# Kernel tuning notes

Hardware: AMD Instinct MI355X
Metric: run time of the kernel (lower is better)

Reference implementation:

```python
import jax, jax.numpy as jnp
from jax import lax
import numpy as np

N, I, O = 64, 8, 8
B = 512
S_EX, S_PHI, S_RHO = 10, 60, 60  # S_phi must equal S_rho (alpha loops feed S_rho-sized h into the GRUs)
N_ACTIONS, N_ROLES = 5, 7


def _gru(x, h, Wih, Whh, bih, bhh):
    # torch.nn.GRUCell math
    gi = x @ Wih.T + bih
    gh = h @ Whh.T + bhh
    ir, iz, inn = jnp.split(gi, 3, axis=-1)
    hr, hz, hn = jnp.split(gh, 3, axis=-1)
    r = jax.nn.sigmoid(ir + hr)
    zg = jax.nn.sigmoid(iz + hz)
    n = jnp.tanh(inn + r * hn)
    return (1.0 - zg) * n + zg * h


def setup_inputs() -> dict:
    key = jax.random.key(0)
    ks = jax.random.split(key, 24)
    f32 = jnp.float32
    z = jax.random.normal(ks[0], (B, N, S_EX), f32)
    dz = jax.random.normal(ks[1], (B, N, S_EX), f32)
    has = (jax.random.uniform(ks[2], (B, N)) < 0.9).astype(f32)
    adj = (jnp.triu(jax.random.uniform(ks[3], (N, N)), 1) > 0.7).astype(jnp.int32)

    def lin(k, o, i):
        return (jax.random.normal(k, (o, i), f32) * np.float32(1.0 / np.sqrt(i)))

    d = dict(z=z, dz=dz, has=has, adj=adj)
    d['Wih_f'] = lin(ks[4], 3 * S_PHI, S_RHO)
    d['Whh_f'] = lin(ks[5], 3 * S_PHI, S_PHI)
    d['bih_f'] = jax.random.normal(ks[6], (3 * S_PHI,), f32) * 0.02
    d['bhh_f'] = jax.random.normal(ks[7], (3 * S_PHI,), f32) * 0.02
    d['Wih_b'] = lin(ks[8], 3 * S_PHI, S_RHO)
    d['Whh_b'] = lin(ks[9], 3 * S_PHI, S_PHI)
    d['bih_b'] = jax.random.normal(ks[10], (3 * S_PHI,), f32) * 0.02
    d['bhh_b'] = jax.random.normal(ks[11], (3 * S_PHI,), f32) * 0.02
    d['Wf'] = lin(ks[12], S_RHO, S_PHI + 2 * S_EX)
    d['bf'] = jax.random.normal(ks[13], (S_RHO,), f32) * 0.02
    d['Wb'] = lin(ks[14], S_RHO, S_PHI + 2 * S_EX)
    d['bb'] = jax.random.normal(ks[15], (S_RHO,), f32) * 0.02
    d['Wa'] = lin(ks[16], N_ACTIONS, 2 * S_PHI)
    d['ba'] = jax.random.normal(ks[17], (N_ACTIONS,), f32) * 0.02
    d['Wc'] = lin(ks[18], 1, 2 * S_PHI)
    d['bc'] = jax.random.normal(ks[19], (1,), f32) * 0.02
    d['Wu'] = lin(ks[20], N_ROLES, 2 * S_RHO)
    d['bu'] = jax.random.normal(ks[21], (N_ROLES,), f32) * 0.02
    return d


def reference(z, dz, has, adj,
              Wih_f, Whh_f, bih_f, bhh_f,
              Wih_b, Whh_b, bih_b, bhh_b,
              Wf, bf, Wb, bb, Wa, ba, Wc, bc, Wu, bu):
    Bn, Nn = has.shape
    dt = z.dtype
    adjf = adj.astype(dt)

    # ---- forward sweep over nodes in ascending order ----
    def fwd_outer(rho, i):
        def inner(h, j):
            hn = _gru(rho[j], h, Wih_f, Whh_f, bih_f, bhh_f)
            blend = adjf[j, i] * has[:, j][:, None]  # edge exists AND source node present
            return h + blend * (hn - h), None
        h, _ = lax.scan(inner, jnp.zeros((Bn, S_PHI), dt), jnp.arange(Nn))
        rho_i = jnp.tanh(jnp.concatenate([h, z[:, i], dz[:, i]], 1) @ Wf.T + bf)
        return rho.at[i].set(rho_i), None

    rho_f, _ = lax.scan(fwd_outer, jnp.zeros((Nn, Bn, S_RHO), dt), jnp.arange(Nn))

    # ---- backward sweep over nodes in descending order ----
    def bwd_outer(rho, i):
        def inner(h, j):
            hn = _gru(rho[j], h, Wih_b, Whh_b, bih_b, bhh_b)
            blend = adjf[i, j] * has[:, j][:, None]  # out-edges of i, visited descending
            return h + blend * (hn - h), None
        h, _ = lax.scan(inner, jnp.zeros((Bn, S_PHI), dt), jnp.arange(Nn - 1, -1, -1))
        rho_i = jnp.concatenate([h, z[:, i], dz[:, i]], 1) @ Wb.T + bb
        return rho.at[i].set(rho_i), None

    rho_b, _ = lax.scan(bwd_outer, jnp.zeros((Nn, Bn, S_RHO), dt), jnp.arange(Nn - 1, -1, -1))

    # ---- aggregate outputs (last O nodes) and inputs (first I nodes) ----
    h = jnp.zeros((Bn, S_RHO), dt)
    for i in range(N - O, N):
        hn = _gru(rho_f[i], h, Wih_f, Whh_f, bih_f, bhh_f)
        h = h + has[:, i][:, None] * (hn - h)
    alpha_f = h
    h = jnp.zeros((Bn, S_RHO), dt)
    for i in reversed(range(I)):
        hn = _gru(rho_b[i], h, Wih_b, Whh_b, bih_b, bhh_b)
        h = h + has[:, i][:, None] * (hn - h)
    alpha_b = h

    ab = jnp.concatenate([alpha_f, alpha_b], 1)
    omega = ab @ Wa.T + ba          # [B, 5]
    value = ab @ Wc.T + bc          # [B, 1]

    feats = jnp.concatenate([rho_f, rho_b], -1)           # [N, B, 2*S_rho]
    psi = jnp.einsum('nbs,rs->brn', feats, Wu) + bu[None, :, None]  # [B, 7, N]
    m = has[:, None, :]
    psi = -60.0 * (1.0 - m) + psi * m  # interpolate(-60, psi, has)

    instr_prob = jax.nn.softmax(omega, axis=1)
    role_prob = jax.nn.softmax(psi, axis=2)
    return instr_prob, role_prob, value
```

## Files before the change

kernel.cpp:

```cpp
#include <hip/hip_runtime.h>
#include <hip/hip_bf16.h>

#define NN 64
#define BATCH 512
#define SP 60
#define SG 180
#define SEX 10
#define CATD 80
#define NA 5
#define NR 7
#define OO 8
#define II 8

typedef unsigned long long u64;
typedef unsigned short u16;
typedef unsigned int u32;
typedef unsigned char u8;

#define OFF_Z     0
#define OFF_DZ    327680
#define OFF_HAS   655360
#define OFF_WIHF  688128
#define OFF_WHHF  698928
#define OFF_BIHF  709728
#define OFF_BHHF  709908
#define OFF_WIHB  710088
#define OFF_WHHB  720888
#define OFF_BIHB  731688
#define OFF_BHHB  731868
#define OFF_WF    732048
#define OFF_BF    736848
#define OFF_WB    736908
#define OFF_BB    741708
#define OFF_WA    741768
#define OFF_BA    742368
#define OFF_WC    742373
#define OFF_BC    742493
#define OFF_WU    742494
#define OFF_BU    743334
#define CONV_TOTAL 743341
#define OFF_FLAG  743342
#define OFF_RHOF  743344
#define OFF_RHOB  (OFF_RHOF + 1966080)
#define OFF_ALF   (OFF_RHOB + 1966080)
#define OFF_ALB   (OFF_ALF + 30720)
#define OUT_TOTAL 232448

typedef _Float16 f16;
typedef _Float16 half2_t __attribute__((ext_vector_type(2)));
typedef _Float16 f16x8 __attribute__((ext_vector_type(8)));
typedef float f32x4 __attribute__((ext_vector_type(4)));

__device__ __forceinline__ float us2f(u16 v){
  return __uint_as_float(((u32)v) << 16);
}
__device__ __forceinline__ u16 f2bf(float f){
  __hip_bfloat16 h = __float2bfloat16(f);
  return *reinterpret_cast<u16*>(&h);
}
__device__ __forceinline__ float rcp_(float x){ return __builtin_amdgcn_rcpf(x); }
__device__ __forceinline__ float sigm(float x){
  return rcp_(1.f + __expf(-x));
}
__device__ __forceinline__ float tanh_(float x){
  float e = __expf(2.f*fabsf(x));
  float t = 1.f - 2.f*rcp_(e + 1.f);
  return copysignf(t, x);
}
__device__ __forceinline__ u32 pack2(float a, float b){
  half2_t h; h[0] = (f16)a; h[1] = (f16)b;
  return __builtin_bit_cast(u32, h);
}
__device__ __forceinline__ float fdot2_(u32 a, u32 b, float c){
  return __builtin_amdgcn_fdot2(__builtin_bit_cast(half2_t, a),
                                __builtin_bit_cast(half2_t, b), c, false);
}
__device__ __forceinline__ f16x8 bc16(uint4 v){ return __builtin_bit_cast(f16x8, v); }
__device__ __forceinline__ f32x4 mfma16(f16x8 a, f16x8 b, f32x4 c){
  return __builtin_amdgcn_mfma_f32_16x16x32_f16(a, b, c, 0, 0, 0);
}

struct HP { uint4 q[8]; };
__device__ __forceinline__ u32 hpc(const HP& p, int k){
  const uint4& v = p.q[k>>2];
  switch(k&3){ case 0: return v.x; case 1: return v.y; case 2: return v.z; default: return v.w; }
}

__device__ __forceinline__ int detect_bf16(const u32* w){
  int f = 0;
  for (int i=0;i<256;i++) f |= (w[i] == 0x3F803F80u) ? 1 : 0;
  return f;
}

__global__ __launch_bounds__(256) void conv_in(
  const void* z, const void* dz, const void* has,
  const void* WihF, const void* WhhF, const void* bihF, const void* bhhF,
  const void* WihB, const void* WhhB, const void* bihB, const void* bhhB,
  const void* Wf_, const void* bf_, const void* Wb_, const void* bb_,
  const void* Wa, const void* ba, const void* Wc, const void* bc,
  const void* Wu, const void* bu, float* ws)
{
  const int isbf = detect_bf16((const u32*)has);
  if (blockIdx.x == 0 && threadIdx.x == 0) ws[OFF_FLAG] = (float)isbf;
  int idx = blockIdx.x*256 + threadIdx.x;
  if (idx >= CONV_TOTAL) return;
  const void* src; int loc;
  if      (idx < OFF_DZ  ){ src=z;    loc=idx-OFF_Z;    }
  else if (idx < OFF_HAS ){ src=dz;   loc=idx-OFF_DZ;   }
  else if (idx < OFF_WIHF){ src=has;  loc=idx-OFF_HAS;  }
  else if (idx < OFF_WHHF){ src=WihF; loc=idx-OFF_WIHF; }
  else if (idx < OFF_BIHF){ src=WhhF; loc=idx-OFF_WHHF; }
  else if (idx < OFF_BHHF){ src=bihF; loc=idx-OFF_BIHF; }
  else if (idx < OFF_WIHB){ src=bhhF; loc=idx-OFF_BHHF; }
  else if (idx < OFF_WHHB){ src=WihB; loc=idx-OFF_WIHB; }
  else if (idx < OFF_BIHB){ src=WhhB; loc=idx-OFF_WHHB; }
  else if (idx < OFF_BHHB){ src=bihB; loc=idx-OFF_BIHB; }
  else if (idx < OFF_WF  ){ src=bhhB; loc=idx-OFF_BHHB; }
  else if (idx < OFF_BF  ){ src=Wf_;  loc=idx-OFF_WF;   }
  else if (idx < OFF_WB  ){ src=bf_;  loc=idx-OFF_BF;   }
  else if (idx < OFF_BB  ){ src=Wb_;  loc=idx-OFF_WB;   }
  else if (idx < OFF_WA  ){ src=bb_;  loc=idx-OFF_BB;   }
  else if (idx < OFF_BA  ){ src=Wa;   loc=idx-OFF_WA;   }
  else if (idx < OFF_WC  ){ src=ba;   loc=idx-OFF_BA;   }
  else if (idx < OFF_BC  ){ src=Wc;   loc=idx-OFF_WC;   }
  else if (idx < OFF_WU  ){ src=bc;   loc=idx-OFF_BC;   }
  else if (idx < OFF_BU  ){ src=Wu;   loc=idx-OFF_WU;   }
  else                    { src=bu;   loc=idx-OFF_BU;   }
  float v = isbf ? us2f(((const u16*)src)[loc]) : ((const float*)src)[loc];
  ws[idx] = v;
}

__global__ __launch_bounds__(256, 4) void dir_kernel(const int* __restrict__ adj,
                                                     float* __restrict__ ws)
{
  const int tid = threadIdx.x;
  const int w   = tid >> 6;
  const int u   = tid & 63;
  const int ml  = u & 15;
  const int q   = u >> 4;
  const int bid = blockIdx.x;
  const int bwd = bid >> 9;
  const int b   = bid & 511;

  const float* Wih  = ws + (bwd ? OFF_WIHB : OFF_WIHF);
  const float* Whh  = ws + (bwd ? OFF_WHHB : OFF_WHHF);
  const float* bih  = ws + (bwd ? OFF_BIHB : OFF_BIHF);
  const float* bhh  = ws + (bwd ? OFF_BHHB : OFF_BHHF);
  const float* Wcat = ws + (bwd ? OFF_WB   : OFF_WF);
  const float* bcat = ws + (bwd ? OFF_BB   : OFF_BF);
  const float* zc   = ws + OFF_Z;
  const float* dzc  = ws + OFF_DZ;
  const float* hasc = ws + OFF_HAS;
  float* rho   = ws + (bwd ? OFF_RHOB : OFF_RHOF);
  float* alpha = ws + (bwd ? OFF_ALB  : OFF_ALF);

  __shared__ uint4 sH4[65][9];
  __shared__ uint4 sRhoPad[8];
  __shared__ uint4 sRhoHist[8][8];
  __shared__ float sRhoOut[NN][SP];
  __shared__ u32 sZp[NN][5];
  __shared__ u32 sDZp[NN][5];
  __shared__ float sHas[NN];
  __shared__ u64 sRowM[NN];
  __shared__ u8 sConsL[NN][64];
  __shared__ int sConsCnt[NN];

  #define ROWB(I) ((char*)&sH4[(I)][0])
  const u32 BIASW = 0x3C000000u;

  {
    if (tid < 64){
      u64 rowm = 0;
      for (int j=0;j<64;j++) rowm |= ((u64)(adj[tid*64+j]!=0))<<j;
      sRowM[tid] = rowm;
      sHas[tid] = hasc[b*NN + tid];
    }
    for (int idx=tid; idx<65*9; idx+=256){
      uint4 v = {0,0,0,0};
      if (idx % 9 == 7) v.w = BIASW;
      ((uint4*)sH4)[idx] = v;
    }
    if (tid < 8){ uint4 v={0,0,0,0}; if (tid==7) v.w = BIASW; sRhoPad[tid]=v; }
    if (tid < 64){ uint4 v={0,0,0,0}; if ((tid&7)==7) v.w = BIASW; ((uint4*)sRhoHist)[tid]=v; }
    for (int idx=tid; idx<NN*5; idx+=256){
      int n2=idx/5, p2=idx%5;
      sZp [n2][p2] = pack2(zc [(size_t)b*NN*SEX + n2*SEX + 2*p2],
                           zc [(size_t)b*NN*SEX + n2*SEX + 2*p2+1]);
      sDZp[n2][p2] = pack2(dzc[(size_t)b*NN*SEX + n2*SEX + 2*p2],
                           dzc[(size_t)b*NN*SEX + n2*SEX + 2*p2+1]);
    }
  }
  __syncthreads();
  if (tid < 64){
    u64 cm = 0;
    if (bwd) for (int i2=0;i2<64;i2++) cm |= ((sRowM[i2]>>tid)&1ULL)<<i2;
    u64 m = bwd ? cm : sRowM[tid];
    int c = 0;
    while (m){ int i2 = (int)__builtin_ctzll(m); m &= m-1; sConsL[tid][c++] = (u8)i2; }
    sConsCnt[tid] = c;
  }

  f16x8 Ar[4], Az[4], Anh[2], Ani[2];
  {
    const int R = 16*w + ml;
    const bool rok = (R < SP);
    #pragma unroll
    for (int kt=0; kt<4; kt++){
      f16x8 vr, vz;
      #pragma unroll
      for (int j=0;j<8;j++){
        const int K = 32*kt + 8*q + j;
        float wr=0.f, wz=0.f;
        if (rok){
          if (K < SP){ wr = Whh[R*SP+K]; wz = Whh[(60+R)*SP+K]; }
          else if (K >= 64 && K < 64+SP){ wr = Wih[R*SP+(K-64)]; wz = Wih[(60+R)*SP+(K-64)]; }
          else if (K == 127){ wr = bhh[R]+bih[R]; wz = bhh[60+R]+bih[60+R]; }
        }
        vr[j]=(f16)wr; vz[j]=(f16)wz;
      }
      Ar[kt]=vr; Az[kt]=vz;
    }
    #pragma unroll
    for (int kt=0; kt<2; kt++){
      f16x8 vn, vi;
      #pragma unroll
      for (int j=0;j<8;j++){
        const int K = 32*kt + 8*q + j;
        float wn=0.f, wi=0.f;
        if (rok){
          if (K < SP){ wn = Whh[(120+R)*SP+K]; wi = Wih[(120+R)*SP+K]; }
          else if (K == 63){ wn = bhh[120+R]; wi = bih[120+R]; }
        }
        vn[j]=(f16)wn; vi[j]=(f16)wi;
      }
      Anh[kt]=vn; Ani[kt]=vi;
    }
  }

  u32 wc[40];
  float bct = 0.f;
  if (w == 0){
    #pragma unroll
    for (int k=0;k<40;k++) wc[k] = pack2(Wcat[u*CATD + 2*k], Wcat[u*CATD + 2*k+1]);
    bct = bcat[u];
  }
  __syncthreads();

  auto gatepass = [&](f16x8 Bh0, f16x8 Bh1, f16x8 Br0, f16x8 Br1,
                      f32x4 Gn, int ci, bool wr, float bl){
    f32x4 Dr={0,0,0,0}, Dz={0,0,0,0}, Dn={0,0,0,0};
    Dr = mfma16(Ar[0], Bh0, Dr); Dr = mfma16(Ar[1], Bh1, Dr);
    Dr = mfma16(Ar[2], Br0, Dr); Dr = mfma16(Ar[3], Br1, Dr);
    Dz = mfma16(Az[0], Bh0, Dz); Dz = mfma16(Az[1], Bh1, Dz);
    Dz = mfma16(Az[2], Br0, Dz); Dz = mfma16(Az[3], Br1, Dz);
    Dn = mfma16(Anh[0], Bh0, Dn); Dn = mfma16(Anh[1], Bh1, Dn);

    char* rp = ROWB(ci) + 32*w + 8*q;
    uint2 h2 = *(uint2*)rp;
    half2_t ha = __builtin_bit_cast(half2_t, h2.x);
    half2_t hb = __builtin_bit_cast(half2_t, h2.y);
    float hold[4] = { (float)ha[0], (float)ha[1], (float)hb[0], (float)hb[1] };
    float hw[4];
    #pragma unroll
    for (int reg=0;reg<4;reg++){
      float r_ = sigm(Dr[reg]);
      float zg = sigm(Dz[reg]);
      float nv = tanh_(Gn[reg] + r_*Dn[reg]);
      float hn_ = (1.f - zg)*nv + zg*hold[reg];
      hw[reg] = (bl != 0.f) ? hn_ : hold[reg];
    }
    if (wr && !(w==3 && q==3)){
      uint2 o; o.x = pack2(hw[0],hw[1]); o.y = pack2(hw[2],hw[3]);
      *(uint2*)rp = o;
    }
  };

  int t = bwd ? 63 : 0;
  const int dt = bwd ? -1 : 1;
  for (int s=0; s<64; s++, t+=dt){
    if (w == 0){
      HP ht;
      { const uint4* _r=(const uint4*)&sH4[t][0];
        #pragma unroll
        for (int _k=0;_k<8;_k++) ht.q[_k]=_r[_k]; }
      float c0 = bct, c1 = 0.f, c2 = 0.f, c3 = 0.f;
      #pragma unroll
      for (int k=0;k<28;k+=4){
        c0 = fdot2_(wc[k],   hpc(ht,k),   c0);
        c1 = fdot2_(wc[k+1], hpc(ht,k+1), c1);
        c2 = fdot2_(wc[k+2], hpc(ht,k+2), c2);
        c3 = fdot2_(wc[k+3], hpc(ht,k+3), c3);
      }
      c0 = fdot2_(wc[28], hpc(ht,28), c0);
      c1 = fdot2_(wc[29], hpc(ht,29), c1);
      #pragma unroll
      for (int p2=0;p2<5;p2++){
        c2 = fdot2_(wc[30+p2], sZp [t][p2], c2);
        c3 = fdot2_(wc[35+p2], sDZp[t][p2], c3);
      }
      float acc = (c0 + c1) + (c2 + c3);
      float rv = bwd ? acc : tanh_(acc);
      if (u < SP){
        sRhoOut[t][u] = rv;
        *(f16*)((char*)&sRhoPad[0] + 2*u) = (f16)rv;
      }
      const int slot = bwd ? t : (t - (NN-OO));
      if (slot >= 0 && slot < 8 && u < SP)
        *(f16*)((char*)&sRhoHist[slot][0] + 2*u) = (f16)rv;
    }
    __syncthreads();

    const float blendT = sHas[t];
    const int cnt = sConsCnt[t];
    if (blendT != 0.f && cnt > 0){
      const f16x8 Br0 = bc16(sRhoPad[q]);
      const f16x8 Br1 = bc16(sRhoPad[4+q]);
      f32x4 Gn={0,0,0,0};
      Gn = mfma16(Ani[0], Br0, Gn);
      Gn = mfma16(Ani[1], Br1, Gn);
      const int np = (cnt + 15) >> 4;
      for (int p=0; p<np; p++){
        const int idxp = 16*p + ml;
        const int ci = (idxp < cnt) ? (int)sConsL[t][idxp] : 64;
        const f16x8 Bh0 = bc16(sH4[ci][q]);
        const f16x8 Bh1 = bc16(sH4[ci][4+q]);
        __syncthreads();
        gatepass(Bh0, Bh1, Br0, Br1, Gn, ci, idxp < cnt, 1.0f);
      }
    }
    __syncthreads();
  }

  for (int idx=tid; idx<NN*SP; idx+=256){
    int n2 = idx/SP, s2 = idx%SP;
    rho[((size_t)n2*BATCH + b)*SP + s2] = sRhoOut[n2][s2];
  }

  for (int s2=0; s2<8; s2++){
    const int i = bwd ? (7 - s2) : (NN - OO + s2);
    const int slot = bwd ? i : (i - (NN-OO));
    const f16x8 Th0 = bc16(sH4[64][q]);
    const f16x8 Th1 = bc16(sH4[64][4+q]);
    const f16x8 Tr0 = bc16(sRhoHist[slot][q]);
    const f16x8 Tr1 = bc16(sRhoHist[slot][4+q]);
    f32x4 Gt={0,0,0,0};
    Gt = mfma16(Ani[0], Tr0, Gt);
    Gt = mfma16(Ani[1], Tr1, Gt);
    __syncthreads();
    gatepass(Th0, Th1, Tr0, Tr1, Gt, 64, ml==0, sHas[i]);
    __syncthreads();
  }
  if (tid < SP) alpha[(size_t)b*SP + tid] = (float)*(const f16*)(ROWB(64) + 2*tid);
  #undef ROWB
}

__global__ __launch_bounds__(256, 1) void head_kernel(float* __restrict__ ws,
                                                      void* __restrict__ outp)
{
  const int b = blockIdx.x;
  const int tid = threadIdx.x;
  const int isbf = (ws[OFF_FLAG] != 0.f);
  const float* hasc   = ws + OFF_HAS;
  const float* WaC    = ws + OFF_WA;
  const float* baC    = ws + OFF_BA;
  const float* WcC    = ws + OFF_WC;
  const float* bcC    = ws + OFF_BC;
  const float* WuC    = ws + OFF_WU;
  const float* buC    = ws + OFF_BU;
  const float* rhoF   = ws + OFF_RHOF;
  const float* rhoB   = ws + OFF_RHOB;
  const float* alphaF = ws + OFF_ALF;
  const float* alphaB = ws + OFF_ALB;

  __shared__ float sF[NN][121];
  __shared__ float sAB[120];
  __shared__ float sWu[NR*120];
  __shared__ float sHasR[NN];
  __shared__ float sPsi[NR][NN];
  __shared__ float sRed[NR][2];
  __shared__ float sOm[NA];

  auto wout = [&](int idx, float v){
    if (isbf) ((u16*)outp)[idx] = f2bf(v);
    else      ((float*)outp)[idx] = v;
  };

  for (int idx=tid; idx<NN*SP; idx+=256){
    int n = idx/SP, s = idx%SP;
    sF[n][s]    = rhoF[((size_t)n*BATCH + b)*SP + s];
    sF[n][60+s] = rhoB[((size_t)n*BATCH + b)*SP + s];
  }
  for (int idx=tid; idx<120; idx+=256)
    sAB[idx] = (idx<60) ? alphaF[(size_t)b*SP + idx] : alphaB[(size_t)b*SP + idx-60];
  for (int idx=tid; idx<NR*120; idx+=256) sWu[idx] = WuC[idx];
  for (int idx=tid; idx<NN; idx+=256) sHasR[idx] = hasc[b*NN + idx];
  __syncthreads();

  for (int idx=tid; idx<NR*NN; idx+=256){
    int r = idx/NN, n = idx%NN;
    float acc = buC[r];
    for (int s=0;s<120;s++) acc += sF[n][s]*sWu[r*120+s];
    sPsi[r][n] = (sHasR[n] != 0.f) ? acc : -60.f;
  }
  if (tid >= 64 && tid < 64+NA){
    int a = tid - 64;
    float acc = baC[a];
    for (int s=0;s<120;s++) acc += sAB[s]*WaC[a*120+s];
    sOm[a] = acc;
  }
  if (tid == 70){
    float acc = bcC[0];
    for (int s=0;s<120;s++) acc += sAB[s]*WcC[s];
    wout(2560 + BATCH*NR*NN + b, acc);
  }
  __syncthreads();

  if (tid < NR){
    float m = -1e30f;
    for (int n=0;n<NN;n++) m = fmaxf(m, sPsi[tid][n]);
    float ssum = 0.f;
    for (int n=0;n<NN;n++) ssum += __expf(sPsi[tid][n]-m);
    sRed[tid][0] = m; sRed[tid][1] = 1.f/ssum;
  }
  if (tid == 8){
    float m = -1e30f;
    for (int a=0;a<NA;a++) m = fmaxf(m, sOm[a]);
    float e[NA]; float ssum = 0.f;
    for (int a=0;a<NA;a++){ e[a] = __expf(sOm[a]-m); ssum += e[a]; }
    for (int a=0;a<NA;a++) wout(b*NA + a, e[a]/ssum);
  }
  __syncthreads();

  for (int idx=tid; idx<NR*NN; idx+=256){
    int r = idx/NN, n = idx%NN;
    float v = __expf(sPsi[r][n]-sRed[r][0]) * sRed[r][1];
    wout(2560 + (size_t)b*NR*NN + idx, v);
  }
}

extern "C" void kernel_launch(void* const* d_in, const int* in_sizes, int n_in,
                              void* d_out, int out_size, void* d_ws, size_t ws_size,
                              hipStream_t stream)
{
  const int* adj = (const int*)d_in[3];
  float* ws = (float*)d_ws;

  conv_in<<<(CONV_TOTAL+255)/256, 256, 0, stream>>>(
      d_in[0], d_in[1], d_in[2],
      d_in[4], d_in[5], d_in[6], d_in[7],
      d_in[8], d_in[9], d_in[10], d_in[11],
      d_in[12], d_in[13], d_in[14], d_in[15],
      d_in[16], d_in[17], d_in[18], d_in[19],
      d_in[20], d_in[21], ws);

  dir_kernel<<<1024, 256, 0, stream>>>(adj, ws);

  head_kernel<<<512, 256, 0, stream>>>(ws, d_out);
}
```

Measured before the change: 281.9 us.

## Split per-node rho projection across all four waves and precompute z/dz term

The z/dz contribution of the concatenated rho projection is now computed for all nodes before the recurrence, spread across all threads, and kept in shared memory. Inside the serial node loop, the h-part dot product is split across the four waves, and wave 0 sums the partials instead of doing the whole 80-wide dot alone. Rho is written straight to global memory each step instead of being staged and copied out at the end. This shortens the serial critical path per step but adds one extra block barrier per step plus a shared partial-sum exchange.

```diff
diff --git a/kernel.cpp b/kernel.cpp
--- a/kernel.cpp
+++ b/kernel.cpp
@@ -78,12 +78,6 @@
 __device__ __forceinline__ f16x8 bc16(uint4 v){ return __builtin_bit_cast(f16x8, v); }
 __device__ __forceinline__ f32x4 mfma16(f16x8 a, f16x8 b, f32x4 c){
   return __builtin_amdgcn_mfma_f32_16x16x32_f16(a, b, c, 0, 0, 0);
-}
-
-struct HP { uint4 q[8]; };
-__device__ __forceinline__ u32 hpc(const HP& p, int k){
-  const uint4& v = p.q[k>>2];
-  switch(k&3){ case 0: return v.x; case 1: return v.y; case 2: return v.z; default: return v.w; }
 }
 
 __device__ __forceinline__ int detect_bf16(const u32* w){
@@ -157,7 +151,8 @@
   __shared__ uint4 sH4[65][9];
   __shared__ uint4 sRhoPad[8];
   __shared__ uint4 sRhoHist[8][8];
-  __shared__ float sRhoOut[NN][SP];
+  __shared__ float sZdc[NN][SP];
+  __shared__ float sPart[4][64];
   __shared__ u32 sZp[NN][5];
   __shared__ u32 sDZp[NN][5];
   __shared__ float sHas[NN];
@@ -198,6 +193,26 @@
     int c = 0;
     while (m){ int i2 = (int)__builtin_ctzll(m); m &= m-1; sConsL[tid][c++] = (u8)i2; }
     sConsCnt[tid] = c;
+  }
+  {
+    const int uu = tid & 63;
+    const int tw = tid >> 6;
+    if (uu < SP){
+      u32 wz[10];
+      #pragma unroll
+      for (int p=0;p<10;p++)
+        wz[p] = pack2(Wcat[uu*CATD + 60 + 2*p], Wcat[uu*CATD + 60 + 2*p + 1]);
+      const float bb0 = bcat[uu];
+      for (int t2=tw; t2<NN; t2+=4){
+        float c = bb0;
+        #pragma unroll
+        for (int p=0;p<5;p++){
+          c = fdot2_(wz[p],   sZp [t2][p], c);
+          c = fdot2_(wz[5+p], sDZp[t2][p], c);
+        }
+        sZdc[t2][uu] = c;
+      }
+    }
   }
 
   f16x8 Ar[4], Az[4], Anh[2], Ani[2];
@@ -210,13 +225,13 @@
       #pragma unroll
       for (int j=0;j<8;j++){
         const int K = 32*kt + 8*q + j;
-        float wr=0.f, wz=0.f;
+        float wr=0.f, wz2=0.f;
         if (rok){
-          if (K < SP){ wr = Whh[R*SP+K]; wz = Whh[(60+R)*SP+K]; }
-          else if (K >= 64 && K < 64+SP){ wr = Wih[R*SP+(K-64)]; wz = Wih[(60+R)*SP+(K-64)]; }
-          else if (K == 127){ wr = bhh[R]+bih[R]; wz = bhh[60+R]+bih[60+R]; }
+          if (K < SP){ wr = Whh[R*SP+K]; wz2 = Whh[(60+R)*SP+K]; }
+          else if (K >= 64 && K < 64+SP){ wr = Wih[R*SP+(K-64)]; wz2 = Wih[(60+R)*SP+(K-64)]; }
+          else if (K == 127){ wr = bhh[R]+bih[R]; wz2 = bhh[60+R]+bih[60+R]; }
         }
-        vr[j]=(f16)wr; vz[j]=(f16)wz;
+        vr[j]=(f16)wr; vz[j]=(f16)wz2;
       }
       Ar[kt]=vr; Az[kt]=vz;
     }
@@ -237,12 +252,11 @@
     }
   }
 
-  u32 wc[40];
-  float bct = 0.f;
-  if (w == 0){
-    #pragma unroll
-    for (int k=0;k<40;k++) wc[k] = pack2(Wcat[u*CATD + 2*k], Wcat[u*CATD + 2*k+1]);
-    bct = bcat[u];
+  u32 wc[8];
+  #pragma unroll
+  for (int k=0;k<8;k++){
+    const int kk = 8*w + k;
+    wc[k] = (kk < 30) ? pack2(Wcat[u*CATD + 2*kk], Wcat[u*CATD + 2*kk + 1]) : 0u;
   }
   __syncthreads();
 
@@ -278,30 +292,25 @@
   int t = bwd ? 63 : 0;
   const int dt = bwd ? -1 : 1;
   for (int s=0; s<64; s++, t+=dt){
+    {
+      const uint4* hr = &sH4[t][0];
+      float cp = 0.f;
+      if (w == 3) cp = (u < SP) ? sZdc[t][u] : 0.f;
+      uint4 ha = hr[2*w];
+      uint4 hb = hr[2*w+1];
+      cp = fdot2_(wc[0], ha.x, cp); cp = fdot2_(wc[1], ha.y, cp);
+      cp = fdot2_(wc[2], ha.z, cp); cp = fdot2_(wc[3], ha.w, cp);
+      cp = fdot2_(wc[4], hb.x, cp); cp = fdot2_(wc[5], hb.y, cp);
+      if (w < 3){ cp = fdot2_(wc[6], hb.z, cp); cp = fdot2_(wc[7], hb.w, cp); }
+      sPart[w][u] = cp;
+    }
+    __syncthreads();
+
     if (w == 0){
-      HP ht;
-      { const uint4* _r=(const uint4*)&sH4[t][0];
-        #pragma unroll
-        for (int _k=0;_k<8;_k++) ht.q[_k]=_r[_k]; }
-      float c0 = bct, c1 = 0.f, c2 = 0.f, c3 = 0.f;
-      #pragma unroll
-      for (int k=0;k<28;k+=4){
-        c0 = fdot2_(wc[k],   hpc(ht,k),   c0);
-        c1 = fdot2_(wc[k+1], hpc(ht,k+1), c1);
-        c2 = fdot2_(wc[k+2], hpc(ht,k+2), c2);
-        c3 = fdot2_(wc[k+3], hpc(ht,k+3), c3);
-      }
-      c0 = fdot2_(wc[28], hpc(ht,28), c0);
-      c1 = fdot2_(wc[29], hpc(ht,29), c1);
-      #pragma unroll
-      for (int p2=0;p2<5;p2++){
-        c2 = fdot2_(wc[30+p2], sZp [t][p2], c2);
-        c3 = fdot2_(wc[35+p2], sDZp[t][p2], c3);
-      }
-      float acc = (c0 + c1) + (c2 + c3);
+      float acc = (sPart[0][u] + sPart[1][u]) + (sPart[2][u] + sPart[3][u]);
       float rv = bwd ? acc : tanh_(acc);
       if (u < SP){
-        sRhoOut[t][u] = rv;
+        rho[((size_t)t*BATCH + b)*SP + u] = rv;
         *(f16*)((char*)&sRhoPad[0] + 2*u) = (f16)rv;
       }
       const int slot = bwd ? t : (t - (NN-OO));
@@ -331,11 +340,6 @@
     __syncthreads();
   }
 
-  for (int idx=tid; idx<NN*SP; idx+=256){
-    int n2 = idx/SP, s2 = idx%SP;
-    rho[((size_t)n2*BATCH + b)*SP + s2] = sRhoOut[n2][s2];
-  }
-
   for (int s2=0; s2<8; s2++){
     const int i = bwd ? (7 - s2) : (NN - OO + s2);
     const int slot = bwd ? i : (i - (NN-OO));
```

New measurement: 268.4 us. -4.8%, faster.
